# Kernel optimization log

Hardware: AMD Instinct MI355X
Metric: run time of the kernel (lower is better)

Reference implementation:

```python
import jax, jax.numpy as jnp
import numpy as np

B, S, D, H = 8, 1024, 768, 12
DH = D // H  # 64


def setup_inputs() -> dict:
    key = jax.random.key(0)
    ks = jax.random.split(key, 7)
    scale = 0.05
    return {
        "sequences": jax.random.normal(ks[0], (B, S, D), dtype=jnp.float32),
        "Wq": jax.random.normal(ks[1], (H, DH, DH), dtype=jnp.float32) * scale,
        "bq": jax.random.normal(ks[2], (H, DH), dtype=jnp.float32) * scale,
        "Wk": jax.random.normal(ks[3], (H, DH, DH), dtype=jnp.float32) * scale,
        "bk": jax.random.normal(ks[4], (H, DH), dtype=jnp.float32) * scale,
        "Wv": jax.random.normal(ks[5], (H, DH, DH), dtype=jnp.float32) * scale,
        "bv": jax.random.normal(ks[6], (H, DH), dtype=jnp.float32) * scale,
    }


def reference(sequences, Wq, bq, Wk, bk, Wv, bv):
    # sequences: [B, S, D]; per-head slice of width DH gets its own Linear.
    b, s, d = sequences.shape
    h, dh = Wq.shape[0], Wq.shape[-1]
    xh = sequences.reshape(b, s, h, dh)  # [B,S,H,DH] head-chunked features
    q = jnp.einsum('bshd,hde->bshe', xh, Wq) + bq  # [B,S,H,DH]
    k = jnp.einsum('bshd,hde->bshe', xh, Wk) + bk
    v = jnp.einsum('bshd,hde->bshe', xh, Wv) + bv
    scores = jnp.einsum('bqhd,bkhd->bhqk', q, k) / jnp.sqrt(jnp.float32(dh))
    weights = jax.nn.softmax(scores, axis=-1)  # [B,H,S,S]
    out = jnp.einsum('bhqk,bkhd->bqhd', weights, v)  # [B,S,H,DH]
    return out.reshape(b, s, d)  # hstack of heads == reshape back to D
```

## Files before the change

### kernel.cpp

```cpp
#include <hip/hip_runtime.h>
#include <hip/hip_bf16.h>
#include <math.h>

constexpr int Bn = 8, Sn = 1024, Dn = 768, Hn = 12, DHn = 64;
constexpr float SQC = 0.42466086f;

typedef __attribute__((ext_vector_type(8))) short bf16x8;
typedef __attribute__((ext_vector_type(4))) float f32x4;

__device__ __forceinline__ unsigned short f2bf(float f) {
    union { float f; unsigned u; } c{f};
    return (unsigned short)((c.u + 0x8000) >> 16);
}
__device__ __forceinline__ unsigned int pk2bf(float a, float b) {
    union { float f; unsigned u; } ca{a}, cb{b};
    return __builtin_amdgcn_perm(cb.u + 0x8000u, ca.u + 0x8000u, 0x07060302u);
}

__global__ __launch_bounds__(256) void prep_kernel(
    const float* __restrict__ Wq, const float* __restrict__ Wk,
    const float* __restrict__ Wv, unsigned short* __restrict__ wt_g)
{
    __shared__ float Ws[64][65];
    const int mh = blockIdx.x;
    const int m  = mh / Hn;
    const int h  = mh % Hn;
    const float* W = (m == 0 ? Wq : (m == 1 ? Wk : Wv)) + (size_t)h * 4096;
    const int t  = threadIdx.x;
    const int r  = t >> 2;
    const int c0 = (t & 3) * 16;
    #pragma unroll
    for (int q4 = 0; q4 < 4; q4++) {
        float4 v = ((const float4*)(W + r * 64 + c0))[q4];
        Ws[r][c0 + 4 * q4 + 0] = v.x;
        Ws[r][c0 + 4 * q4 + 1] = v.y;
        Ws[r][c0 + 4 * q4 + 2] = v.z;
        Ws[r][c0 + 4 * q4 + 3] = v.w;
    }
    __syncthreads();
    const int e  = t >> 2;
    const int d0 = (t & 3) * 16;
    const float sc = (m < 2) ? SQC : 1.0f;
    unsigned short tmp[16];
    #pragma unroll
    for (int j = 0; j < 16; j++) tmp[j] = f2bf(Ws[d0 + j][e] * sc);
    uint4* dst = (uint4*)(wt_g + ((size_t)(mh * 64 + e)) * 64 + d0);
    dst[0] = ((uint4*)tmp)[0];
    dst[1] = ((uint4*)tmp)[1];
}

__global__ __launch_bounds__(256) void attn_kernel(
    const float* __restrict__ x, const unsigned short* __restrict__ wt_g,
    const float* __restrict__ bq, const float* __restrict__ bk,
    const float* __restrict__ bv,
    float* __restrict__ out)
{
    __shared__ unsigned short Xs[64 * 72];
    __shared__ unsigned short Ks[64 * 72];
    __shared__ unsigned short Vt[64 * 72];
    __shared__ unsigned short Pws[4 * 32 * 72];

    const int blk = blockIdx.x;
    const int xcd = blk & 7;
    const int idx = blk >> 3;
    const int bh  = xcd * 12 + (idx % 12);
    const int qt  = idx / 12;
    const int t    = threadIdx.x;
    const int w    = t >> 6;
    const int lane = t & 63;
    const int l    = lane & 15;
    const int quad = lane >> 4;
    const int sr   = t >> 2;
    const int sc0  = (t & 3) * 16;

    const int b = bh / Hn, h = bh % Hn;
    unsigned short* Pw = Pws + w * 32 * 72;

    bf16x8 wk[2], wv[2];
    {
        const unsigned short* kp = wt_g + ((size_t)((1 * Hn + h) * 64 + w * 16 + l)) * 64 + quad * 8;
        const unsigned short* vp = wt_g + ((size_t)((2 * Hn + h) * 64 + w * 16 + l)) * 64 + quad * 8;
        uint4 a0 = *(const uint4*)kp;  uint4 a1 = *(const uint4*)(kp + 32);
        uint4 b0 = *(const uint4*)vp;  uint4 b1 = *(const uint4*)(vp + 32);
        wk[0] = *(bf16x8*)&a0; wk[1] = *(bf16x8*)&a1;
        wv[0] = *(bf16x8*)&b0; wv[1] = *(bf16x8*)&b1;
    }
    float4 bkv = *(const float4*)(bk + h * 64 + w * 16 + quad * 4);
    bkv.x *= SQC; bkv.y *= SQC; bkv.z *= SQC; bkv.w *= SQC;
    const float bvl = bv[h * 64 + w * 16 + l];

    bf16x8 qf[2][2];
    {
        bf16x8 xq[2][2];
        #pragma unroll
        for (int st = 0; st < 2; st++) {
            const float* xp = x + ((size_t)(b * Sn + qt * 128 + w * 32 + st * 16 + l) * Dn
                                   + h * 64 + quad * 8);
            #pragma unroll
            for (int kc = 0; kc < 2; kc++) {
                float4 v0 = *(const float4*)(xp + kc * 32);
                float4 v1 = *(const float4*)(xp + kc * 32 + 4);
                unsigned int tmp[4] = {pk2bf(v0.x, v0.y), pk2bf(v0.z, v0.w),
                                       pk2bf(v1.x, v1.y), pk2bf(v1.z, v1.w)};
                xq[st][kc] = *(bf16x8*)tmp;
            }
        }
        #pragma unroll
        for (int nt = 0; nt < 4; nt++) {
            const unsigned short* wp = wt_g + ((size_t)((0 * Hn + h) * 64 + nt * 16 + l)) * 64 + quad * 8;
            uint4 a0 = *(const uint4*)wp;
            uint4 a1 = *(const uint4*)(wp + 32);
            bf16x8 wa0 = *(bf16x8*)&a0, wa1 = *(bf16x8*)&a1;
            float4 bqv = *(const float4*)(bq + h * 64 + nt * 16 + quad * 4);
            #pragma unroll
            for (int st = 0; st < 2; st++) {
                f32x4 acc = (f32x4){bqv.x * SQC, bqv.y * SQC, bqv.z * SQC, bqv.w * SQC};
                acc = __builtin_amdgcn_mfma_f32_16x16x32_bf16(wa0, xq[st][0], acc, 0, 0, 0);
                acc = __builtin_amdgcn_mfma_f32_16x16x32_bf16(wa1, xq[st][1], acc, 0, 0, 0);
                *(uint2*)&Pw[(st * 16 + l) * 72 + nt * 16 + quad * 4] =
                    make_uint2(pk2bf(acc[0], acc[1]), pk2bf(acc[2], acc[3]));
            }
        }
        __asm__ volatile("s_waitcnt lgkmcnt(0)" ::: "memory");
        #pragma unroll
        for (int st = 0; st < 2; st++) {
            qf[st][0] = *(bf16x8*)&Pw[(st * 16 + l) * 72 + quad * 8];
            qf[st][1] = *(bf16x8*)&Pw[(st * 16 + l) * 72 + 32 + quad * 8];
        }
    }

    f32x4 Oa[2][4];
    #pragma unroll
    for (int st = 0; st < 2; st++)
        #pragma unroll
        for (int nt = 0; nt < 4; nt++) Oa[st][nt] = (f32x4){0.f, 0.f, 0.f, 0.f};
    float ps[2] = {0.f, 0.f};

    for (int kt = 0; kt < 16; kt++) {
        __syncthreads();
        {
            const float* xrow = x + ((size_t)(b * Sn + kt * 64 + sr) * Dn + h * 64 + sc0);
            unsigned int tmp[8];
            #pragma unroll
            for (int q4 = 0; q4 < 4; q4++) {
                float4 v = ((const float4*)xrow)[q4];
                tmp[2 * q4 + 0] = pk2bf(v.x, v.y);
                tmp[2 * q4 + 1] = pk2bf(v.z, v.w);
            }
            *(uint4*)&Xs[sr * 72 + sc0]     = ((uint4*)tmp)[0];
            *(uint4*)&Xs[sr * 72 + sc0 + 8] = ((uint4*)tmp)[1];
        }
        __syncthreads();

        {
            bf16x8 xf[4][2];
            #pragma unroll
            for (int nt = 0; nt < 4; nt++)
                #pragma unroll
                for (int kc = 0; kc < 2; kc++)
                    xf[nt][kc] = *(bf16x8*)&Xs[(nt * 16 + l) * 72 + kc * 32 + quad * 8];

            #pragma unroll
            for (int nt = 0; nt < 4; nt++) {
                f32x4 ak = (f32x4){bkv.x, bkv.y, bkv.z, bkv.w};
                ak = __builtin_amdgcn_mfma_f32_16x16x32_bf16(wk[0], xf[nt][0], ak, 0, 0, 0);
                ak = __builtin_amdgcn_mfma_f32_16x16x32_bf16(wk[1], xf[nt][1], ak, 0, 0, 0);
                *(uint2*)&Ks[(nt * 16 + l) * 72 + w * 16 + quad * 4] =
                    make_uint2(pk2bf(ak[0], ak[1]), pk2bf(ak[2], ak[3]));
                f32x4 av = (f32x4){bvl, bvl, bvl, bvl};
                av = __builtin_amdgcn_mfma_f32_16x16x32_bf16(xf[nt][0], wv[0], av, 0, 0, 0);
                av = __builtin_amdgcn_mfma_f32_16x16x32_bf16(xf[nt][1], wv[1], av, 0, 0, 0);
                *(uint2*)&Vt[(w * 16 + l) * 72 + nt * 16 + quad * 4] =
                    make_uint2(pk2bf(av[0], av[1]), pk2bf(av[2], av[3]));
            }
        }
        __syncthreads();

        #pragma unroll
        for (int nt = 0; nt < 4; nt++) {
            bf16x8 kf0 = *(bf16x8*)&Ks[(nt * 16 + l) * 72 + quad * 8];
            bf16x8 kf1 = *(bf16x8*)&Ks[(nt * 16 + l) * 72 + 32 + quad * 8];
            #pragma unroll
            for (int st = 0; st < 2; st++) {
                f32x4 s = (f32x4){0.f, 0.f, 0.f, 0.f};
                s = __builtin_amdgcn_mfma_f32_16x16x32_bf16(kf0, qf[st][0], s, 0, 0, 0);
                s = __builtin_amdgcn_mfma_f32_16x16x32_bf16(kf1, qf[st][1], s, 0, 0, 0);
                float p0 = exp2f(s[0]), p1 = exp2f(s[1]);
                float p2 = exp2f(s[2]), p3 = exp2f(s[3]);
                ps[st] += (p0 + p1) + (p2 + p3);
                *(uint2*)&Pw[(st * 16 + l) * 72 + nt * 16 + quad * 4] =
                    make_uint2(pk2bf(p0, p1), pk2bf(p2, p3));
            }
        }
        __asm__ volatile("s_waitcnt lgkmcnt(0)" ::: "memory");

        bf16x8 pf[2][2];
        #pragma unroll
        for (int st = 0; st < 2; st++) {
            pf[st][0] = *(bf16x8*)&Pw[(st * 16 + l) * 72 + quad * 8];
            pf[st][1] = *(bf16x8*)&Pw[(st * 16 + l) * 72 + 32 + quad * 8];
        }

        #pragma unroll
        for (int nt = 0; nt < 4; nt++) {
            bf16x8 vf0 = *(bf16x8*)&Vt[(nt * 16 + l) * 72 + quad * 8];
            bf16x8 vf1 = *(bf16x8*)&Vt[(nt * 16 + l) * 72 + 32 + quad * 8];
            #pragma unroll
            for (int st = 0; st < 2; st++) {
                Oa[st][nt] = __builtin_amdgcn_mfma_f32_16x16x32_bf16(pf[st][0], vf0, Oa[st][nt], 0, 0, 0);
                Oa[st][nt] = __builtin_amdgcn_mfma_f32_16x16x32_bf16(pf[st][1], vf1, Oa[st][nt], 0, 0, 0);
            }
        }
    }

    #pragma unroll
    for (int st = 0; st < 2; st++) {
        ps[st] += __shfl_xor(ps[st], 16, 64);
        ps[st] += __shfl_xor(ps[st], 32, 64);
    }

    #pragma unroll
    for (int st = 0; st < 2; st++) {
        float inv[4];
        #pragma unroll
        for (int r = 0; r < 4; r++) inv[r] = 1.0f / __shfl(ps[st], quad * 4 + r, 64);
        #pragma unroll
        for (int nt = 0; nt < 4; nt++)
            #pragma unroll
            for (int r = 0; r < 4; r++) {
                int srow = qt * 128 + w * 32 + st * 16 + quad * 4 + r;
                out[(size_t)(b * Sn + srow) * Dn + h * 64 + nt * 16 + l] = Oa[st][nt][r] * inv[r];
            }
    }
}

extern "C" void kernel_launch(void* const* d_in, const int* in_sizes, int n_in,
                              void* d_out, int out_size, void* d_ws, size_t ws_size,
                              hipStream_t stream) {
    const float* x  = (const float*)d_in[0];
    const float* Wq = (const float*)d_in[1];
    const float* bq = (const float*)d_in[2];
    const float* Wk = (const float*)d_in[3];
    const float* bk = (const float*)d_in[4];
    const float* Wv = (const float*)d_in[5];
    const float* bv = (const float*)d_in[6];
    float* out = (float*)d_out;

    unsigned short* wt_g = (unsigned short*)d_ws;

    hipLaunchKernelGGL(prep_kernel, dim3(3 * Hn), dim3(256), 0, stream,
                       Wq, Wk, Wv, wt_g);
    hipLaunchKernelGGL(attn_kernel, dim3(Bn * Hn * 8), dim3(256), 0, stream,
                       x, wt_g, bq, bk, bv, out);
}
```

Before: 169.7 us.

## Precompute K and V projections once in separate kernel, prefetch in attention

Before this change, every query-tile block recomputed the K and V projections for all key tiles, so the projection work was repeated eight times per head. A new projection kernel now computes K (row-major) and V (transposed) once per head and writes them to workspace in bf16. The attention kernel then streams these tiles with a register prefetch of the next tile, which also drops one barrier per iteration. In exchange there is an extra kernel launch and a round trip of K and V through global memory. The weight fragments for Q, K and V are now gathered straight from the fp32 weights with strided loads instead of a separate transpose prep kernel.

```diff
diff --git a/kernel.cpp b/kernel.cpp
--- a/kernel.cpp
+++ b/kernel.cpp
@@ -3,6 +3,7 @@
 #include <math.h>
 
 constexpr int Bn = 8, Sn = 1024, Dn = 768, Hn = 12, DHn = 64;
+constexpr int QKV_ELEMS = Bn * Hn * Sn * DHn;
 constexpr float SQC = 0.42466086f;
 
 typedef __attribute__((ext_vector_type(8))) short bf16x8;
@@ -17,45 +18,111 @@
     return __builtin_amdgcn_perm(cb.u + 0x8000u, ca.u + 0x8000u, 0x07060302u);
 }
 
-__global__ __launch_bounds__(256) void prep_kernel(
-    const float* __restrict__ Wq, const float* __restrict__ Wk,
-    const float* __restrict__ Wv, unsigned short* __restrict__ wt_g)
+__device__ __forceinline__ bf16x8 wfrag(const float* __restrict__ W,
+                                        int e, int kc, int quad, float sc) {
+    const float* p = W + (size_t)(kc * 32 + quad * 8) * 64 + e;
+    unsigned int tmp[4];
+    #pragma unroll
+    for (int j = 0; j < 4; j++)
+        tmp[j] = pk2bf(p[(2 * j) * 64] * sc, p[(2 * j + 1) * 64] * sc);
+    return *(bf16x8*)tmp;
+}
+
+__global__ __launch_bounds__(256) void proj_kernel(
+    const float* __restrict__ x,
+    const float* __restrict__ Wk, const float* __restrict__ bk,
+    const float* __restrict__ Wv, const float* __restrict__ bv,
+    unsigned short* __restrict__ k_ws, unsigned short* __restrict__ vt_ws)
 {
-    __shared__ float Ws[64][65];
-    const int mh = blockIdx.x;
-    const int m  = mh / Hn;
-    const int h  = mh % Hn;
-    const float* W = (m == 0 ? Wq : (m == 1 ? Wk : Wv)) + (size_t)h * 4096;
-    const int t  = threadIdx.x;
-    const int r  = t >> 2;
-    const int c0 = (t & 3) * 16;
-    #pragma unroll
-    for (int q4 = 0; q4 < 4; q4++) {
-        float4 v = ((const float4*)(W + r * 64 + c0))[q4];
-        Ws[r][c0 + 4 * q4 + 0] = v.x;
-        Ws[r][c0 + 4 * q4 + 1] = v.y;
-        Ws[r][c0 + 4 * q4 + 2] = v.z;
-        Ws[r][c0 + 4 * q4 + 3] = v.w;
-    }
+    __shared__ unsigned short Xs[64 * 72];
+    __shared__ unsigned short ObK[64 * 72];
+    __shared__ unsigned short ObV[64 * 72];
+
+    const int blk  = blockIdx.x;
+    const int tile = blk & 15;
+    const int bh   = blk >> 4;
+    const int h    = bh % Hn;
+    const int b    = bh / Hn;
+    const int t    = threadIdx.x;
+    const int w    = t >> 6;
+    const int lane = t & 63;
+    const int l    = lane & 15;
+    const int quad = lane >> 4;
+    const int sr   = t >> 2;
+    const int sc0  = (t & 3) * 16;
+    const int s0   = tile * 64;
+
+    {
+        const float* xrow = x + ((size_t)(b * Sn + s0 + sr) * Dn + h * 64 + sc0);
+        unsigned int tmp[8];
+        #pragma unroll
+        for (int q4 = 0; q4 < 4; q4++) {
+            float4 v = ((const float4*)xrow)[q4];
+            tmp[2 * q4 + 0] = pk2bf(v.x, v.y);
+            tmp[2 * q4 + 1] = pk2bf(v.z, v.w);
+        }
+        *(uint4*)&Xs[sr * 72 + sc0]     = ((uint4*)tmp)[0];
+        *(uint4*)&Xs[sr * 72 + sc0 + 8] = ((uint4*)tmp)[1];
+    }
+
+    const int e = w * 16 + l;
+    bf16x8 wk[2], wv[2];
+    #pragma unroll
+    for (int kc = 0; kc < 2; kc++) {
+        wk[kc] = wfrag(Wk + (size_t)h * 4096, e, kc, quad, SQC);
+        wv[kc] = wfrag(Wv + (size_t)h * 4096, e, kc, quad, 1.0f);
+    }
+    float4 bkv = *(const float4*)(bk + h * 64 + w * 16 + quad * 4);
+    bkv.x *= SQC; bkv.y *= SQC; bkv.z *= SQC; bkv.w *= SQC;
+    const float bvl = bv[h * 64 + e];
+
     __syncthreads();
-    const int e  = t >> 2;
-    const int d0 = (t & 3) * 16;
-    const float sc = (m < 2) ? SQC : 1.0f;
-    unsigned short tmp[16];
-    #pragma unroll
-    for (int j = 0; j < 16; j++) tmp[j] = f2bf(Ws[d0 + j][e] * sc);
-    uint4* dst = (uint4*)(wt_g + ((size_t)(mh * 64 + e)) * 64 + d0);
-    dst[0] = ((uint4*)tmp)[0];
-    dst[1] = ((uint4*)tmp)[1];
+
+    bf16x8 xf[4][2];
+    #pragma unroll
+    for (int nt = 0; nt < 4; nt++)
+        #pragma unroll
+        for (int kc = 0; kc < 2; kc++)
+            xf[nt][kc] = *(bf16x8*)&Xs[(nt * 16 + l) * 72 + kc * 32 + quad * 8];
+
+    #pragma unroll
+    for (int nt = 0; nt < 4; nt++) {
+        f32x4 ak = (f32x4){bkv.x, bkv.y, bkv.z, bkv.w};
+        ak = __builtin_amdgcn_mfma_f32_16x16x32_bf16(wk[0], xf[nt][0], ak, 0, 0, 0);
+        ak = __builtin_amdgcn_mfma_f32_16x16x32_bf16(wk[1], xf[nt][1], ak, 0, 0, 0);
+        *(uint2*)&ObK[(nt * 16 + l) * 72 + w * 16 + quad * 4] =
+            make_uint2(pk2bf(ak[0], ak[1]), pk2bf(ak[2], ak[3]));
+        f32x4 av = (f32x4){bvl, bvl, bvl, bvl};
+        av = __builtin_amdgcn_mfma_f32_16x16x32_bf16(xf[nt][0], wv[0], av, 0, 0, 0);
+        av = __builtin_amdgcn_mfma_f32_16x16x32_bf16(xf[nt][1], wv[1], av, 0, 0, 0);
+        *(uint2*)&ObV[(w * 16 + l) * 72 + nt * 16 + quad * 4] =
+            make_uint2(pk2bf(av[0], av[1]), pk2bf(av[2], av[3]));
+    }
+    __syncthreads();
+
+    {
+        uint4 a  = *(uint4*)&ObK[sr * 72 + sc0];
+        uint4 b4 = *(uint4*)&ObK[sr * 72 + sc0 + 8];
+        unsigned short* dst = k_ws + (size_t)(bh * Sn + s0 + sr) * 64 + sc0;
+        ((uint4*)dst)[0] = a;
+        *(uint4*)(dst + 8) = b4;
+    }
+    {
+        uint4 a  = *(uint4*)&ObV[sr * 72 + sc0];
+        uint4 b4 = *(uint4*)&ObV[sr * 72 + sc0 + 8];
+        unsigned short* dst = vt_ws + (size_t)bh * 64 * Sn + (size_t)sr * Sn + s0 + sc0;
+        ((uint4*)dst)[0] = a;
+        *(uint4*)(dst + 8) = b4;
+    }
 }
 
 __global__ __launch_bounds__(256) void attn_kernel(
-    const float* __restrict__ x, const unsigned short* __restrict__ wt_g,
-    const float* __restrict__ bq, const float* __restrict__ bk,
-    const float* __restrict__ bv,
+    const float* __restrict__ x,
+    const float* __restrict__ Wq, const float* __restrict__ bq,
+    const unsigned short* __restrict__ k_ws,
+    const unsigned short* __restrict__ vt_ws,
     float* __restrict__ out)
 {
-    __shared__ unsigned short Xs[64 * 72];
     __shared__ unsigned short Ks[64 * 72];
     __shared__ unsigned short Vt[64 * 72];
     __shared__ unsigned short Pws[4 * 32 * 72];
@@ -74,20 +141,9 @@
     const int sc0  = (t & 3) * 16;
 
     const int b = bh / Hn, h = bh % Hn;
+    const size_t base  = (size_t)bh * Sn * 64;
+    const size_t vbase = (size_t)bh * 64 * Sn;
     unsigned short* Pw = Pws + w * 32 * 72;
-
-    bf16x8 wk[2], wv[2];
-    {
-        const unsigned short* kp = wt_g + ((size_t)((1 * Hn + h) * 64 + w * 16 + l)) * 64 + quad * 8;
-        const unsigned short* vp = wt_g + ((size_t)((2 * Hn + h) * 64 + w * 16 + l)) * 64 + quad * 8;
-        uint4 a0 = *(const uint4*)kp;  uint4 a1 = *(const uint4*)(kp + 32);
-        uint4 b0 = *(const uint4*)vp;  uint4 b1 = *(const uint4*)(vp + 32);
-        wk[0] = *(bf16x8*)&a0; wk[1] = *(bf16x8*)&a1;
-        wv[0] = *(bf16x8*)&b0; wv[1] = *(bf16x8*)&b1;
-    }
-    float4 bkv = *(const float4*)(bk + h * 64 + w * 16 + quad * 4);
-    bkv.x *= SQC; bkv.y *= SQC; bkv.z *= SQC; bkv.w *= SQC;
-    const float bvl = bv[h * 64 + w * 16 + l];
 
     bf16x8 qf[2][2];
     {
@@ -107,10 +163,8 @@
         }
         #pragma unroll
         for (int nt = 0; nt < 4; nt++) {
-            const unsigned short* wp = wt_g + ((size_t)((0 * Hn + h) * 64 + nt * 16 + l)) * 64 + quad * 8;
-            uint4 a0 = *(const uint4*)wp;
-            uint4 a1 = *(const uint4*)(wp + 32);
-            bf16x8 wa0 = *(bf16x8*)&a0, wa1 = *(bf16x8*)&a1;
+            bf16x8 wa0 = wfrag(Wq + (size_t)h * 4096, nt * 16 + l, 0, quad, SQC);
+            bf16x8 wa1 = wfrag(Wq + (size_t)h * 4096, nt * 16 + l, 1, quad, SQC);
             float4 bqv = *(const float4*)(bq + h * 64 + nt * 16 + quad * 4);
             #pragma unroll
             for (int st = 0; st < 2; st++) {
@@ -136,45 +190,34 @@
         for (int nt = 0; nt < 4; nt++) Oa[st][nt] = (f32x4){0.f, 0.f, 0.f, 0.f};
     float ps[2] = {0.f, 0.f};
 
+    uint4 kpre0, kpre1, vpre0, vpre1;
+    {
+        const unsigned short* kp = k_ws + base + (size_t)sr * 64 + sc0;
+        kpre0 = *(const uint4*)kp;
+        kpre1 = *(const uint4*)(kp + 8);
+        const unsigned short* vp = vt_ws + vbase + (size_t)sr * Sn + sc0;
+        vpre0 = *(const uint4*)vp;
+        vpre1 = *(const uint4*)(vp + 8);
+    }
+
     for (int kt = 0; kt < 16; kt++) {
         __syncthreads();
         {
-            const float* xrow = x + ((size_t)(b * Sn + kt * 64 + sr) * Dn + h * 64 + sc0);
-            unsigned int tmp[8];
-            #pragma unroll
-            for (int q4 = 0; q4 < 4; q4++) {
-                float4 v = ((const float4*)xrow)[q4];
-                tmp[2 * q4 + 0] = pk2bf(v.x, v.y);
-                tmp[2 * q4 + 1] = pk2bf(v.z, v.w);
-            }
-            *(uint4*)&Xs[sr * 72 + sc0]     = ((uint4*)tmp)[0];
-            *(uint4*)&Xs[sr * 72 + sc0 + 8] = ((uint4*)tmp)[1];
+            *(uint4*)&Ks[sr * 72 + sc0]     = kpre0;
+            *(uint4*)&Ks[sr * 72 + sc0 + 8] = kpre1;
+            *(uint4*)&Vt[sr * 72 + sc0]     = vpre0;
+            *(uint4*)&Vt[sr * 72 + sc0 + 8] = vpre1;
         }
         __syncthreads();
 
-        {
-            bf16x8 xf[4][2];
-            #pragma unroll
-            for (int nt = 0; nt < 4; nt++)
-                #pragma unroll
-                for (int kc = 0; kc < 2; kc++)
-                    xf[nt][kc] = *(bf16x8*)&Xs[(nt * 16 + l) * 72 + kc * 32 + quad * 8];
-
-            #pragma unroll
-            for (int nt = 0; nt < 4; nt++) {
-                f32x4 ak = (f32x4){bkv.x, bkv.y, bkv.z, bkv.w};
-                ak = __builtin_amdgcn_mfma_f32_16x16x32_bf16(wk[0], xf[nt][0], ak, 0, 0, 0);
-                ak = __builtin_amdgcn_mfma_f32_16x16x32_bf16(wk[1], xf[nt][1], ak, 0, 0, 0);
-                *(uint2*)&Ks[(nt * 16 + l) * 72 + w * 16 + quad * 4] =
-                    make_uint2(pk2bf(ak[0], ak[1]), pk2bf(ak[2], ak[3]));
-                f32x4 av = (f32x4){bvl, bvl, bvl, bvl};
-                av = __builtin_amdgcn_mfma_f32_16x16x32_bf16(xf[nt][0], wv[0], av, 0, 0, 0);
-                av = __builtin_amdgcn_mfma_f32_16x16x32_bf16(xf[nt][1], wv[1], av, 0, 0, 0);
-                *(uint2*)&Vt[(w * 16 + l) * 72 + nt * 16 + quad * 4] =
-                    make_uint2(pk2bf(av[0], av[1]), pk2bf(av[2], av[3]));
-            }
-        }
-        __syncthreads();
+        if (kt + 1 < 16) {
+            const unsigned short* kp = k_ws + base + (size_t)((kt + 1) * 64 + sr) * 64 + sc0;
+            kpre0 = *(const uint4*)kp;
+            kpre1 = *(const uint4*)(kp + 8);
+            const unsigned short* vp = vt_ws + vbase + (size_t)sr * Sn + (kt + 1) * 64 + sc0;
+            vpre0 = *(const uint4*)vp;
+            vpre1 = *(const uint4*)(vp + 8);
+        }
 
         #pragma unroll
         for (int nt = 0; nt < 4; nt++) {
@@ -218,7 +261,6 @@
         ps[st] += __shfl_xor(ps[st], 16, 64);
         ps[st] += __shfl_xor(ps[st], 32, 64);
     }
-
     #pragma unroll
     for (int st = 0; st < 2; st++) {
         float inv[4];
@@ -246,10 +288,11 @@
     const float* bv = (const float*)d_in[6];
     float* out = (float*)d_out;
 
-    unsigned short* wt_g = (unsigned short*)d_ws;
-
-    hipLaunchKernelGGL(prep_kernel, dim3(3 * Hn), dim3(256), 0, stream,
-                       Wq, Wk, Wv, wt_g);
+    unsigned short* k_ws  = (unsigned short*)d_ws;
+    unsigned short* vt_ws = k_ws + QKV_ELEMS;
+
+    hipLaunchKernelGGL(proj_kernel, dim3(Bn * Hn * 16), dim3(256), 0, stream,
+                       x, Wk, bk, Wv, bv, k_ws, vt_ws);
     hipLaunchKernelGGL(attn_kernel, dim3(Bn * Hn * 8), dim3(256), 0, stream,
-                       x, wt_g, bq, bk, bv, out);
-}
+                       x, Wq, bq, k_ws, vt_ws, out);
+}
```

After: 140.8 us. -17.0%, faster.
